# Kernel tuning notes

Hardware: AMD Instinct MI355X
Metric: run time of the kernel (lower is better)

## Reference

```python
import jax, jax.numpy as jnp
import numpy as np

D_MODEL = 1024
N_HEADS = 16
D_FF = 4096
B = 8
S_TGT = 1024
S_SRC = 1024


def layer_norm(x, g, b, eps=1e-5):
    mu = jnp.mean(x, axis=-1, keepdims=True)
    var = jnp.mean(jnp.square(x - mu), axis=-1, keepdims=True)
    return (x - mu) * jax.lax.rsqrt(var + eps) * g + b


def mha(q_in, k_in, v_in, Wq, bq, Wk, bk, Wv, bv, Wo, bo, mask):
    Bq, Sq, D = q_in.shape
    hd = D // N_HEADS

    def split(t):
        return t.reshape(t.shape[0], t.shape[1], N_HEADS, hd).transpose(0, 2, 1, 3)

    Q = split(q_in @ Wq + bq)   # [B,H,Sq,hd]
    K = split(k_in @ Wk + bk)   # [B,H,Sk,hd]
    V = split(v_in @ Wv + bv)
    scores = jnp.einsum('bhqd,bhkd->bhqk', Q, K) / jnp.sqrt(jnp.float32(hd))
    scores = jnp.where(mask, scores, jnp.float32(-1e9))
    attn = jax.nn.softmax(scores, axis=-1)
    out = jnp.einsum('bhqk,bhkd->bhqd', attn, V)
    out = out.transpose(0, 2, 1, 3).reshape(Bq, Sq, D)
    return out @ Wo + bo


def setup_inputs() -> dict:
    key = jax.random.key(0)
    ks = jax.random.split(key, 32)
    s = 0.02
    inp = {
        'x': jax.random.normal(ks[0], (B, S_TGT, D_MODEL), dtype=jnp.float32),
        'encoder_output': jax.random.normal(ks[1], (B, S_SRC, D_MODEL), dtype=jnp.float32),
        'tgt_mask': jnp.tril(jnp.ones((S_TGT, S_TGT), dtype=bool))[None, None],
        'src_mask': jnp.ones((1, 1, S_TGT, S_SRC), dtype=bool),
    }
    i = 2
    for p in ('sa', 'ca'):
        for w in ('Wq', 'Wk', 'Wv', 'Wo'):
            inp[f'{p}_{w}'] = jax.random.normal(ks[i], (D_MODEL, D_MODEL), dtype=jnp.float32) * s
            inp[f'{p}_b{w[1].lower()}'] = jnp.zeros((D_MODEL,), dtype=jnp.float32)
            i += 1
    inp['ff_W1'] = jax.random.normal(ks[i], (D_MODEL, D_FF), dtype=jnp.float32) * s; i += 1
    inp['ff_b1'] = jnp.zeros((D_FF,), dtype=jnp.float32)
    inp['ff_W2'] = jax.random.normal(ks[i], (D_FF, D_MODEL), dtype=jnp.float32) * s; i += 1
    inp['ff_b2'] = jnp.zeros((D_MODEL,), dtype=jnp.float32)
    for n in ('ln1', 'ln2', 'ln3'):
        inp[f'{n}_g'] = jnp.ones((D_MODEL,), dtype=jnp.float32)
        inp[f'{n}_b'] = jnp.zeros((D_MODEL,), dtype=jnp.float32)
    return inp


def reference(x, encoder_output, tgt_mask, src_mask,
              sa_Wq, sa_bq, sa_Wk, sa_bk, sa_Wv, sa_bv, sa_Wo, sa_bo,
              ca_Wq, ca_bq, ca_Wk, ca_bk, ca_Wv, ca_bv, ca_Wo, ca_bo,
              ff_W1, ff_b1, ff_W2, ff_b2,
              ln1_g, ln1_b, ln2_g, ln2_b, ln3_g, ln3_b):
    # masked self-attention + residual + LN (dropout = identity in eval mode)
    attn = mha(x, x, x, sa_Wq, sa_bq, sa_Wk, sa_bk, sa_Wv, sa_bv, sa_Wo, sa_bo, tgt_mask)
    x = layer_norm(x + attn, ln1_g, ln1_b)
    # cross-attention to encoder output
    cross = mha(x, encoder_output, encoder_output,
                ca_Wq, ca_bq, ca_Wk, ca_bk, ca_Wv, ca_bv, ca_Wo, ca_bo, src_mask)
    x = layer_norm(x + cross, ln2_g, ln2_b)
    # position-wise FFN: Linear -> ReLU -> Linear
    ff = jax.nn.relu(x @ ff_W1 + ff_b1) @ ff_W2 + ff_b2
    x = layer_norm(x + ff, ln3_g, ln3_b)
    return x
```

## Files before the change

kernel.cpp:

```cpp
#include <hip/hip_runtime.h>
#include <math.h>

typedef __attribute__((ext_vector_type(8))) short short8;
typedef __attribute__((ext_vector_type(4))) short short4v;
typedef __attribute__((ext_vector_type(4))) float floatx4;
typedef __attribute__((ext_vector_type(16))) float floatx16;

__device__ inline float bf2f(unsigned short h) {
    unsigned int u = ((unsigned int)h) << 16;
    float f;
    __builtin_memcpy(&f, &u, 4);
    return f;
}
__device__ inline unsigned short f2bf(float f) {
    unsigned int u;
    __builtin_memcpy(&u, &f, 4);
    u = (u + 0x7fffu + ((u >> 16) & 1u)) >> 16;
    return (unsigned short)u;
}
__device__ inline unsigned int f2u(float f) {
    return __builtin_bit_cast(unsigned int, f);
}
__device__ inline float exp2_raw(float x) {
    float r;
    asm("v_exp_f32 %0, %1" : "=v"(r) : "v"(x));
    return r;
}

__device__ inline void gld_lds16(const unsigned short* g, unsigned short* l) {
    __builtin_amdgcn_global_load_lds(
        (const __attribute__((address_space(1))) unsigned int*)g,
        (__attribute__((address_space(3))) unsigned int*)l, 16, 0, 0);
}

__global__ __launch_bounds__(256) void detect_dtype(
    const unsigned short* __restrict__ x, int* __restrict__ flag) {
    __shared__ int s[4];
    int bad = 0;
    for (int i = threadIdx.x; i < 8192; i += 256) {
        float v = bf2f(x[i]);
        if (!(fabsf(v) <= 1.0e4f)) bad = 1;
    }
    unsigned long long b = __ballot(bad);
    int wave = threadIdx.x >> 6;
    if ((threadIdx.x & 63) == 0) s[wave] = (b != 0ULL) ? 1 : 0;
    __syncthreads();
    if (threadIdx.x == 0) flag[0] = s[0] | s[1] | s[2] | s[3];
}

__global__ __launch_bounds__(256) void to_bf16_kernel(
    const void* __restrict__ in, unsigned short* __restrict__ out,
    const int* __restrict__ flag, int n8) {
    int fl = flag[0];
    int i = blockIdx.x * 256 + threadIdx.x;
    if (i >= n8) return;
    size_t off = (size_t)i * 8;
    if (fl) {
        floatx4 f0 = *(const floatx4*)((const float*)in + off);
        floatx4 f1 = *(const floatx4*)((const float*)in + off + 4);
        short8 v;
#pragma unroll
        for (int j = 0; j < 4; j++) {
            v[j] = (short)f2bf(f0[j]);
            v[4 + j] = (short)f2bf(f1[j]);
        }
        *(short8*)(out + off) = v;
    } else {
        *(short8*)(out + off) = *(const short8*)((const unsigned short*)in + off);
    }
}

__global__ __launch_bounds__(256) void transpose_any(
    const void* __restrict__ in, unsigned short* __restrict__ out,
    int rows, int cols, const int* __restrict__ flag) {
    int fl = flag ? flag[0] : 0;
    __shared__ unsigned short t[32][33];
    int tx = threadIdx.x & 31, ty = threadIdx.x >> 5;
    int c0 = blockIdx.x * 32, r0 = blockIdx.y * 32;
    size_t base = (size_t)blockIdx.z * rows * cols;
#pragma unroll
    for (int k = 0; k < 4; k++) {
        size_t idx = base + (size_t)(r0 + ty + k * 8) * cols + c0 + tx;
        t[ty + k * 8][tx] = fl ? f2bf(((const float*)in)[idx])
                               : ((const unsigned short*)in)[idx];
    }
    __syncthreads();
#pragma unroll
    for (int k = 0; k < 4; k++)
        out[base + (size_t)(c0 + ty + k * 8) * rows + r0 + tx] = t[tx][ty + k * 8];
}

struct Ptr8 { const void* p[8]; };
__global__ __launch_bounds__(256) void transpose8(
    Ptr8 in, unsigned short* __restrict__ out, const int* __restrict__ flag) {
    int fl = flag[0];
    __shared__ unsigned short t[32][33];
    const void* src = in.p[blockIdx.z];
    unsigned short* dst = out + (size_t)blockIdx.z * 1024 * 1024;
    int tx = threadIdx.x & 31, ty = threadIdx.x >> 5;
    int c0 = blockIdx.x * 32, r0 = blockIdx.y * 32;
#pragma unroll
    for (int k = 0; k < 4; k++) {
        size_t idx = (size_t)(r0 + ty + k * 8) * 1024 + c0 + tx;
        t[ty + k * 8][tx] = fl ? f2bf(((const float*)src)[idx])
                               : ((const unsigned short*)src)[idx];
    }
    __syncthreads();
#pragma unroll
    for (int k = 0; k < 4; k++)
        dst[(size_t)(c0 + ty + k * 8) * 1024 + r0 + tx] = t[tx][ty + k * 8];
}

__device__ inline void stage_half(const unsigned short* __restrict__ G, int ldk,
                                  int grow, int gcol, unsigned short* ldsb,
                                  int tid) {
    int s0 = tid, s1 = tid + 512;
    int r0 = s0 >> 3, c0 = ((s0 & 7) ^ (r0 & 7)) << 3;
    int r1 = s1 >> 3, c1 = ((s1 & 7) ^ (r1 & 7)) << 3;
    gld_lds16(&G[(size_t)(grow + r0) * ldk + gcol + c0], &ldsb[s0 * 8]);
    gld_lds16(&G[(size_t)(grow + r1) * ldk + gcol + c1], &ldsb[s1 * 8]);
}

template <int BN_, int EPI>
__global__ __launch_bounds__(512) void gemm8(
    const unsigned short* __restrict__ A, const unsigned short* __restrict__ Bt,
    const void* __restrict__ b0, const void* __restrict__ b1,
    const void* __restrict__ b2, unsigned short* __restrict__ C0,
    unsigned short* __restrict__ C1, unsigned short* __restrict__ C2,
    int M, int N, int K, const int* __restrict__ flag) {
    constexpr int NR = BN_ / 64;
    constexpr int WNT = BN_ / 4;
    constexpr int ASZ = 16384;
    constexpr int BSZ = BN_ * 64;
    __shared__ alignas(16) unsigned short lds[2 * ASZ + 2 * BSZ];

    const int tid = threadIdx.x;
    const int lane = tid & 63, wave = tid >> 6;
    const int quad = lane >> 4, l16 = lane & 15, x7 = l16 & 7;
    const int wm = wave >> 2, wn = wave & 3;
    const int bm = blockIdx.x * 256, bn = blockIdx.y * BN_;
    const int NT = K >> 6;

    floatx4 acc[8][NR];
#pragma unroll
    for (int i = 0; i < 8; ++i)
#pragma unroll
        for (int j = 0; j < NR; ++j) acc[i][j] = (floatx4){0.f, 0.f, 0.f, 0.f};

    stage_half(A, K, bm, 0, lds, tid);
    stage_half(A, K, bm + 128, 0, lds + 8192, tid);
    stage_half(Bt, K, bn, 0, lds + 2 * ASZ, tid);
    if (BN_ == 256) stage_half(Bt, K, bn + 128, 0, lds + 2 * ASZ + 8192, tid);
    asm volatile("s_waitcnt vmcnt(0)" ::: "memory");
    __builtin_amdgcn_s_barrier();

    short8 bfr[NR][2], afr[2][2][2];

    for (int it = 0; it < NT; ++it) {
        unsigned short* const Ac = lds + (it & 1) * ASZ;
        unsigned short* const Bc = lds + 2 * ASZ + (it & 1) * BSZ;
        unsigned short* const An = lds + ((it + 1) & 1) * ASZ;
        unsigned short* const Bn = lds + 2 * ASZ + ((it + 1) & 1) * BSZ;
        const bool more = (it + 1 < NT);
        if (more) {
            const int kn = (it + 1) << 6;
            stage_half(A, K, bm, kn, An, tid);
            stage_half(A, K, bm + 128, kn, An + 8192, tid);
            stage_half(Bt, K, bn, kn, Bn, tid);
            if (BN_ == 256) stage_half(Bt, K, bn + 128, kn, Bn + 8192, tid);
        }
#pragma unroll
        for (int ni = 0; ni < NR; ++ni)
#pragma unroll
            for (int ks = 0; ks < 2; ++ks)
                bfr[ni][ks] = *(const short8*)&Bc[
                    (wn * WNT + ni * 16 + l16) * 64 +
                    ((((ks << 2) + quad) ^ x7) << 3)];
#pragma unroll
        for (int m2 = 0; m2 < 2; ++m2)
#pragma unroll
            for (int ks = 0; ks < 2; ++ks)
                afr[0][m2][ks] = *(const short8*)&Ac[
                    (wm * 128 + m2 * 16 + l16) * 64 +
                    ((((ks << 2) + quad) ^ x7) << 3)];
#pragma unroll
        for (int q = 0; q < 4; ++q) {
            if (q < 3) {
#pragma unroll
                for (int m2 = 0; m2 < 2; ++m2)
#pragma unroll
                    for (int ks = 0; ks < 2; ++ks)
                        afr[(q + 1) & 1][m2][ks] = *(const short8*)&Ac[
                            (wm * 128 + ((q + 1) * 2 + m2) * 16 + l16) * 64 +
                            ((((ks << 2) + quad) ^ x7) << 3)];
            }
            __builtin_amdgcn_s_setprio(1);
#pragma unroll
            for (int m2 = 0; m2 < 2; ++m2)
#pragma unroll
                for (int ni = 0; ni < NR; ++ni) {
                    acc[q * 2 + m2][ni] = __builtin_amdgcn_mfma_f32_16x16x32_bf16(
                        bfr[ni][0], afr[q & 1][m2][0], acc[q * 2 + m2][ni], 0, 0, 0);
                    acc[q * 2 + m2][ni] = __builtin_amdgcn_mfma_f32_16x16x32_bf16(
                        bfr[ni][1], afr[q & 1][m2][1], acc[q * 2 + m2][ni], 0, 0, 0);
                }
            __builtin_amdgcn_s_setprio(0);
        }
        if (more) {
            asm volatile("s_waitcnt vmcnt(0)" ::: "memory");
            __builtin_amdgcn_s_barrier();
        }
    }

    const int fl = flag[0];
    const void* bp = b0;
    unsigned short* Cp = C0;
    int mode = 0;
    int cb = bn;
    if (EPI == 1) mode = 1;
    if (EPI == 4) mode = 2;
    if (EPI == 2) {
        int ch = bn >> 10;
        cb = bn & 1023;
        bp = (ch == 0) ? b0 : (ch == 1) ? b1 : b2;
        Cp = (ch == 0) ? C0 : (ch == 1) ? C1 : C2;
        mode = (ch == 0) ? 2 : (ch == 1) ? 3 : 4;
    }
    if (EPI == 3) {
        int ch = bn >> 10;
        cb = bn & 1023;
        bp = (ch == 0) ? b0 : b1;
        Cp = (ch == 0) ? C0 : C1;
        mode = (ch == 0) ? 3 : 4;
    }

    if (mode == 4) {
#pragma unroll
        for (int ni = 0; ni < NR; ++ni) {
            const int colb = cb + wn * WNT + ni * 16 + quad * 4;
            float b4[4];
            if (fl) {
                floatx4 t = *(const floatx4*)&((const float*)bp)[colb];
#pragma unroll
                for (int r = 0; r < 4; ++r) b4[r] = t[r];
            } else {
                short4v t = *(const short4v*)&((const unsigned short*)bp)[colb];
#pragma unroll
                for (int r = 0; r < 4; ++r) b4[r] = bf2f((unsigned short)t[r]);
            }
            const int hh = colb >> 6, dd = colb & 63;
#pragma unroll
            for (int mi = 0; mi < 8; ++mi) {
                const int row = bm + wm * 128 + mi * 16 + l16;
                const int b_ = row >> 10, s_ = row & 1023;
#pragma unroll
                for (int r = 0; r < 4; ++r) {
                    float v = acc[mi][ni][r] + b4[r];
                    Cp[(((size_t)b_ * 16 + hh) * 64 + dd + r) * 1024 + s_] = f2bf(v);
                }
            }
        }
    } else {
        constexpr int SLOTS = WNT / 8;
        constexpr int SMASK = SLOTS - 1;
        __syncthreads();
        unsigned short* W2 = lds + wave * (128 * WNT);
#pragma unroll
        for (int ni = 0; ni < NR; ++ni) {
            const int colb = cb + wn * WNT + ni * 16 + quad * 4;
            float b4[4];
            if (fl) {
                floatx4 t = *(const floatx4*)&((const float*)bp)[colb];
#pragma unroll
                for (int r = 0; r < 4; ++r) b4[r] = t[r];
            } else {
                short4v t = *(const short4v*)&((const unsigned short*)bp)[colb];
#pragma unroll
                for (int r = 0; r < 4; ++r) b4[r] = bf2f((unsigned short)t[r]);
            }
            const int cslot = ni * 2 + (quad >> 1);
            const int chalf = quad & 1;
#pragma unroll
            for (int mi = 0; mi < 8; ++mi) {
                const int r = mi * 16 + l16;
                short4v pk;
#pragma unroll
                for (int rr = 0; rr < 4; ++rr) {
                    float v = acc[mi][ni][rr] + b4[rr];
                    if (mode == 1) v = fmaxf(v, 0.f);
                    if (mode == 2) v *= 0.18033688f;
                    pk[rr] = (short)f2bf(v);
                }
                *(short4v*)&W2[r * WNT + ((cslot ^ (r & SMASK)) << 3) +
                               (chalf << 2)] = pk;
            }
        }
        const int lslot = lane & SMASK;
        const int lrow = lane / SLOTS;
        constexpr int RPP = 64 / SLOTS;
#pragma unroll
        for (int p = 0; p < 128 / RPP; ++p) {
            const int r = p * RPP + lrow;
            short8 v = *(const short8*)&W2[r * WNT + ((lslot ^ (r & SMASK)) << 3)];
            const int colg = cb + wn * WNT + (lslot << 3);
            const int rowg = bm + wm * 128 + r;
            if (mode <= 1) {
                *(short8*)&Cp[(size_t)rowg * N + colg] = v;
            } else {
                const int b_ = rowg >> 10, s_ = rowg & 1023;
                const int hh2 = colg >> 6, dd2 = colg & 63;
                *(short8*)&Cp[((((size_t)b_ * 16 + hh2) * 1024) + s_) * 64 + dd2] = v;
            }
        }
    }
}

template <int CAUSAL>
__global__ __launch_bounds__(256) void attn_kernel(
    const unsigned short* __restrict__ Q, const unsigned short* __restrict__ K,
    const unsigned short* __restrict__ Vt, unsigned short* __restrict__ O,
    int Skv) {
    __shared__ alignas(16) unsigned short Ks[2][512 * 8];
    __shared__ alignas(16) unsigned short Vs[2][512 * 8];
    const int S = 1024;
    int tid = threadIdx.x, wave = tid >> 6, lane = tid & 63;
    int h = lane >> 5, l31 = lane & 31;
    int fid = blockIdx.y * 8 + blockIdx.x;
    int bh = fid & 127;
    int qt = fid >> 7;
    if (CAUSAL) qt = 7 - qt;
    const int qb = qt * 128 + wave * 32;
    const unsigned short* Qp = Q + (size_t)bh * S * 64;
    const unsigned short* Kp = K + (size_t)bh * Skv * 64;
    const unsigned short* Vp = Vt + (size_t)bh * 64 * Skv;

    short8 qf[4];
#pragma unroll
    for (int t = 0; t < 4; t++)
        qf[t] = *(const short8*)&Qp[(qb + l31) * 64 + t * 16 + h * 8];

    floatx16 o[2];
#pragma unroll
    for (int dn = 0; dn < 2; dn++)
#pragma unroll
        for (int rr = 0; rr < 16; rr++) o[dn][rr] = 0.f;
    float m = -1e30f, l = 0.f;
    const int kend = CAUSAL ? (qt + 1) * 128 : Skv;
    const int nch = kend >> 6;

    int sr0 = tid >> 3, sc0 = (tid & 7) ^ (sr0 & 7);
    int sr1 = (tid + 256) >> 3, sc1 = ((tid + 256) & 7) ^ (sr1 & 7);

    auto stageKV = [&](int kb, int b) {
        gld_lds16(&Kp[(size_t)(kb + sr0) * 64 + sc0 * 8], &Ks[b][tid * 8]);
        gld_lds16(&Kp[(size_t)(kb + sr1) * 64 + sc1 * 8], &Ks[b][(tid + 256) * 8]);
        gld_lds16(&Vp[(size_t)sr0 * Skv + kb + sc0 * 8], &Vs[b][tid * 8]);
        gld_lds16(&Vp[(size_t)sr1 * Skv + kb + sc1 * 8], &Vs[b][(tid + 256) * 8]);
    };

    stageKV(0, 0);
    asm volatile("s_waitcnt vmcnt(0)" ::: "memory");
    __builtin_amdgcn_s_barrier();

    for (int ic = 0; ic < nch; ++ic) {
        const int kb = ic << 6, cur = ic & 1;
        const unsigned short* Ksc = Ks[cur];
        const unsigned short* Vsc = Vs[cur];
        if (ic + 1 < nch) stageKV(kb + 64, cur ^ 1);

        const bool act = !CAUSAL || (kb <= qb + 31);
        if (act) {
            floatx16 st[2];
            __builtin_amdgcn_s_setprio(1);
#pragma unroll
            for (int kg = 0; kg < 2; kg++) {
                const int row = kg * 32 + l31, r7 = row & 7;
                floatx16 z;
#pragma unroll
                for (int rr = 0; rr < 16; rr++) z[rr] = 0.f;
#pragma unroll
                for (int t = 0; t < 4; t++) {
                    short8 kf = *(const short8*)&Ksc[
                        (row * 8 + ((2 * t + h) ^ r7)) * 8];
                    z = __builtin_amdgcn_mfma_f32_32x32x16_bf16(kf, qf[t], z,
                                                                0, 0, 0);
                }
                st[kg] = z;
            }
            __builtin_amdgcn_s_setprio(0);

            if (CAUSAL && (kb + 63 > qb)) {
#pragma unroll
                for (int kg = 0; kg < 2; kg++)
#pragma unroll
                    for (int rr = 0; rr < 16; rr++) {
                        int key = kb + kg * 32 + (rr & 3) + 8 * (rr >> 2) + 4 * h;
                        if (key > qb + l31) st[kg][rr] = -1e30f;
                    }
            }
            float mx[16];
#pragma unroll
            for (int rr = 0; rr < 16; rr++) mx[rr] = fmaxf(st[0][rr], st[1][rr]);
#pragma unroll
            for (int s2 = 8; s2 > 0; s2 >>= 1)
#pragma unroll
                for (int rr = 0; rr < s2; rr++)
                    mx[rr] = fmaxf(mx[rr], mx[rr + s2]);
            float smax = fmaxf(mx[0], __shfl_xor(mx[0], 32));
            float mi = m;
            if (!__all(smax <= m + 8.f)) {
                mi = fmaxf(m, smax);
                float alpha = exp2_raw(m - mi);
                l *= alpha;
#pragma unroll
                for (int dn = 0; dn < 2; dn++)
#pragma unroll
                    for (int rr = 0; rr < 16; rr++) o[dn][rr] *= alpha;
                m = mi;
            }
#pragma unroll
            for (int kg = 0; kg < 2; kg++)
#pragma unroll
                for (int rr = 0; rr < 16; rr++)
                    st[kg][rr] = exp2_raw(st[kg][rr] - mi);
            float sm[16];
#pragma unroll
            for (int rr = 0; rr < 16; rr++) sm[rr] = st[0][rr] + st[1][rr];
#pragma unroll
            for (int s2 = 8; s2 > 0; s2 >>= 1)
#pragma unroll
                for (int rr = 0; rr < s2; rr++) sm[rr] += sm[rr + s2];
            l += sm[0] + __shfl_xor(sm[0], 32);

            unsigned int pd[2][4][2];
#pragma unroll
            for (int kg = 0; kg < 2; kg++)
#pragma unroll
                for (int g = 0; g < 4; g++)
#pragma unroll
                    for (int i = 0; i < 2; i++)
                        pd[kg][g][i] = __builtin_amdgcn_perm(
                            f2u(st[kg][4 * g + 2 * i + 1]),
                            f2u(st[kg][4 * g + 2 * i]), 0x07060302u);

            __builtin_amdgcn_s_setprio(1);
#pragma unroll
            for (int kg = 0; kg < 2; kg++)
#pragma unroll
                for (int kt = 0; kt < 2; kt++) {
                    unsigned int dw[4];
#pragma unroll
                    for (int i = 0; i < 2; i++) {
                        unsigned int a = pd[kg][2 * kt][i];
                        unsigned int b_ = pd[kg][2 * kt + 1][i];
                        unsigned int ax = (unsigned int)__shfl_xor((int)a, 32);
                        unsigned int bx = (unsigned int)__shfl_xor((int)b_, 32);
                        dw[i] = h ? bx : a;
                        dw[2 + i] = h ? b_ : ax;
                    }
                    short8 pf;
                    __builtin_memcpy(&pf, dw, 16);
#pragma unroll
                    for (int dn = 0; dn < 2; dn++) {
                        const int row = dn * 32 + l31, r7 = row & 7;
                        short8 vf = *(const short8*)&Vsc[
                            (row * 8 + ((kg * 4 + 2 * kt + h) ^ r7)) * 8];
                        o[dn] = __builtin_amdgcn_mfma_f32_32x32x16_bf16(
                            vf, pf, o[dn], 0, 0, 0);
                    }
                }
            __builtin_amdgcn_s_setprio(0);
        }

        if (ic + 1 < nch) {
            asm volatile("s_waitcnt vmcnt(0)" ::: "memory");
            __builtin_amdgcn_s_barrier();
        }
    }

    int b = bh >> 4, hh = bh & 15;
    float inv = 1.0f / l;
    size_t orow = ((size_t)(b * S + qb + l31)) * 1024 + hh * 64;
#pragma unroll
    for (int dn = 0; dn < 2; dn++)
#pragma unroll
        for (int g = 0; g < 4; g++) {
            short4v p4;
#pragma unroll
            for (int r = 0; r < 4; r++)
                p4[r] = (short)f2bf(o[dn][4 * g + r] * inv);
            *(short4v*)&O[orow + dn * 32 + 8 * g + 4 * h] = p4;
        }
}

template <int AEXT, int OEXT>
__global__ __launch_bounds__(256) void add_ln_kernel(
    const void* __restrict__ A, const unsigned short* __restrict__ Bv,
    const void* __restrict__ g, const void* __restrict__ be,
    void* __restrict__ out, const int* __restrict__ flag) {
    int fl = flag[0];
    __shared__ float red[2][4];
    int row = blockIdx.x, tid = threadIdx.x;
    size_t base = (size_t)row * 1024;
    int c = tid * 4;
    float v[4], sum = 0.f, ss = 0.f;
    if (AEXT && fl) {
        floatx4 af = *(const floatx4*)&((const float*)A)[base + c];
#pragma unroll
        for (int k = 0; k < 4; k++) v[k] = af[k];
    } else {
        short4v av = *(const short4v*)&((const unsigned short*)A)[base + c];
#pragma unroll
        for (int k = 0; k < 4; k++) v[k] = bf2f((unsigned short)av[k]);
    }
    short4v bv = *(const short4v*)&Bv[base + c];
#pragma unroll
    for (int k = 0; k < 4; k++) {
        v[k] += bf2f((unsigned short)bv[k]);
        sum += v[k];
        ss += v[k] * v[k];
    }
#pragma unroll
    for (int off = 1; off < 64; off <<= 1) {
        sum += __shfl_xor(sum, off);
        ss += __shfl_xor(ss, off);
    }
    int wave = tid >> 6, lane = tid & 63;
    if (lane == 0) {
        red[0][wave] = sum;
        red[1][wave] = ss;
    }
    __syncthreads();
    sum = red[0][0] + red[0][1] + red[0][2] + red[0][3];
    ss = red[1][0] + red[1][1] + red[1][2] + red[1][3];
    float mu = sum * (1.0f / 1024.0f);
    float var = ss * (1.0f / 1024.0f) - mu * mu;
    float rstd = rsqrtf(var + 1e-5f);
#pragma unroll
    for (int k = 0; k < 4; k++) {
        float gv = fl ? ((const float*)g)[c + k]
                      : bf2f(((const unsigned short*)g)[c + k]);
        float bev = fl ? ((const float*)be)[c + k]
                       : bf2f(((const unsigned short*)be)[c + k]);
        float y = (v[k] - mu) * rstd * gv + bev;
        if (OEXT && fl)
            ((float*)out)[base + c + k] = y;
        else
            ((unsigned short*)out)[base + c + k] = f2bf(y);
    }
}

extern "C" void kernel_launch(void* const* d_in, const int* in_sizes, int n_in,
                              void* d_out, int out_size, void* d_ws, size_t ws_size,
                              hipStream_t stream) {
    const int M = 8192;
    typedef const void* cvp;
    cvp x = d_in[0];
    cvp enc = d_in[1];
    cvp saWq = d_in[4], sabq = d_in[5];
    cvp saWk = d_in[6], sabk = d_in[7];
    cvp saWv = d_in[8], sabv = d_in[9];
    cvp saWo = d_in[10], sabo = d_in[11];
    cvp caWq = d_in[12], cabq = d_in[13];
    cvp caWk = d_in[14], cabk = d_in[15];
    cvp caWv = d_in[16], cabv = d_in[17];
    cvp caWo = d_in[18], cabo = d_in[19];
    cvp ffW1 = d_in[20], ffb1 = d_in[21];
    cvp ffW2 = d_in[22], ffb2 = d_in[23];
    cvp ln1g = d_in[24], ln1b = d_in[25];
    cvp ln2g = d_in[26], ln2b = d_in[27];
    cvp ln3g = d_in[28], ln3b = d_in[29];

    char* ws = (char*)d_ws;
    const size_t MB = 1024 * 1024;
    typedef unsigned short* up;
    up wt_sa_qkv = (up)(ws + 0);
    up wt_sa_o   = (up)(ws + 6 * MB);
    up wt_ca_q   = (up)(ws + 8 * MB);
    up wt_ca_kv  = (up)(ws + 10 * MB);
    up wt_ca_o   = (up)(ws + 14 * MB);
    up wtff1     = (up)(ws + 16 * MB);
    up wtff2     = (up)(ws + 24 * MB);
    up Qb  = (up)(ws + 32 * MB);
    up Kb  = (up)(ws + 48 * MB);
    up Vtb = (up)(ws + 64 * MB);
    up xb  = (up)(ws + 80 * MB);
    up Hb  = (up)(ws + 32 * MB);
    up Ob  = (up)(ws + 96 * MB);
    up Pb  = (up)(ws + 112 * MB);
    up x1  = (up)(ws + 128 * MB);
    up x2  = (up)(ws + 144 * MB);
    up encb = (up)(ws + 144 * MB);
    int* flag = (int*)(ws + 160 * MB);

    dim3 blk(256), blk5(512);
    detect_dtype<<<1, blk, 0, stream>>>((const unsigned short*)x, flag);

    to_bf16_kernel<<<4096, blk, 0, stream>>>(x, xb, flag, M * 1024 / 8);
    to_bf16_kernel<<<4096, blk, 0, stream>>>(enc, encb, flag, M * 1024 / 8);

    Ptr8 w8;
    w8.p[0] = saWq; w8.p[1] = saWk; w8.p[2] = saWv; w8.p[3] = saWo;
    w8.p[4] = caWq; w8.p[5] = caWk; w8.p[6] = caWv; w8.p[7] = caWo;
    transpose8<<<dim3(32, 32, 8), blk, 0, stream>>>(w8, (up)(ws + 0), flag);
    transpose_any<<<dim3(128, 32, 1), blk, 0, stream>>>(ffW1, wtff1, 1024, 4096, flag);
    transpose_any<<<dim3(32, 128, 1), blk, 0, stream>>>(ffW2, wtff2, 4096, 1024, flag);

    gemm8<256, 2><<<dim3(32, 12), blk5, 0, stream>>>(
        xb, wt_sa_qkv, sabq, sabk, sabv, Qb, Kb, Vtb, M, 3072, 1024, flag);
    attn_kernel<1><<<dim3(8, 128), blk, 0, stream>>>(Qb, Kb, Vtb, Ob, 1024);
    gemm8<128, 0><<<dim3(32, 8), blk5, 0, stream>>>(
        Ob, wt_sa_o, sabo, nullptr, nullptr, Pb, nullptr, nullptr, M, 1024, 1024, flag);
    add_ln_kernel<1, 0><<<dim3(8192), blk, 0, stream>>>(x, Pb, ln1g, ln1b, x1, flag);

    gemm8<128, 4><<<dim3(32, 8), blk5, 0, stream>>>(
        x1, wt_ca_q, cabq, nullptr, nullptr, Qb, nullptr, nullptr, M, 1024, 1024, flag);
    gemm8<256, 3><<<dim3(32, 8), blk5, 0, stream>>>(
        encb, wt_ca_kv, cabk, cabv, nullptr, Kb, Vtb, nullptr, M, 2048, 1024, flag);
    attn_kernel<0><<<dim3(8, 128), blk, 0, stream>>>(Qb, Kb, Vtb, Ob, 1024);
    gemm8<128, 0><<<dim3(32, 8), blk5, 0, stream>>>(
        Ob, wt_ca_o, cabo, nullptr, nullptr, Pb, nullptr, nullptr, M, 1024, 1024, flag);
    add_ln_kernel<0, 0><<<dim3(8192), blk, 0, stream>>>(x1, Pb, ln2g, ln2b, x2, flag);

    gemm8<256, 1><<<dim3(32, 16), blk5, 0, stream>>>(
        x2, wtff1, ffb1, nullptr, nullptr, Hb, nullptr, nullptr, M, 4096, 1024, flag);
    gemm8<128, 0><<<dim3(32, 8), blk5, 0, stream>>>(
        Hb, wtff2, ffb2, nullptr, nullptr, Pb, nullptr, nullptr, M, 1024, 4096, flag);
    add_ln_kernel<0, 1><<<dim3(8192), blk, 0, stream>>>(x2, Pb, ln3g, ln3b, d_out, flag);
}
```

Before: 703.4 us.

## Add 128x128 gemm4 for N=1024 GEMMs, MFMA row-sum in attention, merge bf16 casts

Adds a new 256-thread 128x128-tile GEMM with 16x16x32 MFMAs and uses it for the four N=1024 projections. The goal is a larger grid (512 blocks instead of 256) to fill more CUs. The attention kernel computes the softmax row sum with MFMAs against a ones vector instead of a shuffle reduction, and flattens the max reduction tree. The two input bf16 conversions are merged into a single launch. Costs include extra MFMA work for the sum and a smaller per-block tile, which means less data reuse.

```diff
diff --git a/kernel.cpp b/kernel.cpp
--- a/kernel.cpp
+++ b/kernel.cpp
@@ -48,10 +48,13 @@
     if (threadIdx.x == 0) flag[0] = s[0] | s[1] | s[2] | s[3];
 }
 
-__global__ __launch_bounds__(256) void to_bf16_kernel(
-    const void* __restrict__ in, unsigned short* __restrict__ out,
+__global__ __launch_bounds__(256) void to_bf16_2(
+    const void* __restrict__ inA, const void* __restrict__ inB,
+    unsigned short* __restrict__ outA, unsigned short* __restrict__ outB,
     const int* __restrict__ flag, int n8) {
     int fl = flag[0];
+    const void* in = blockIdx.z ? inB : inA;
+    unsigned short* out = blockIdx.z ? outB : outA;
     int i = blockIdx.x * 256 + threadIdx.x;
     if (i >= n8) return;
     size_t off = (size_t)i * 8;
@@ -311,6 +314,134 @@
                 const int hh2 = colg >> 6, dd2 = colg & 63;
                 *(short8*)&Cp[((((size_t)b_ * 16 + hh2) * 1024) + s_) * 64 + dd2] = v;
             }
+        }
+    }
+}
+
+__device__ inline void stage128(const unsigned short* __restrict__ G, int ldk,
+                                int grow, int gcol, unsigned short* ldsb,
+                                int tid) {
+#pragma unroll
+    for (int p = 0; p < 4; ++p) {
+        int s = p * 256 + tid;
+        int r = s >> 3, c = ((s & 7) ^ (r & 7)) << 3;
+        gld_lds16(&G[(size_t)(grow + r) * ldk + gcol + c], &ldsb[s * 8]);
+    }
+}
+
+template <int EPI>
+__global__ __launch_bounds__(256) void gemm4(
+    const unsigned short* __restrict__ A, const unsigned short* __restrict__ Bt,
+    const void* __restrict__ bias, unsigned short* __restrict__ C,
+    int M, int N, int K, const int* __restrict__ flag) {
+    constexpr int TSZ = 8192;
+    __shared__ alignas(16) unsigned short lds[4 * TSZ];
+
+    const int tid = threadIdx.x;
+    const int lane = tid & 63, wave = tid >> 6;
+    const int quad = lane >> 4, l16 = lane & 15, x7 = l16 & 7;
+    const int wm = wave >> 1, wn = wave & 1;
+    const int bm = blockIdx.x * 128, bn = blockIdx.y * 128;
+    const int NT = K >> 6;
+
+    floatx4 acc[4][4];
+#pragma unroll
+    for (int i = 0; i < 4; ++i)
+#pragma unroll
+        for (int j = 0; j < 4; ++j) acc[i][j] = (floatx4){0.f, 0.f, 0.f, 0.f};
+
+    stage128(A, K, bm, 0, lds, tid);
+    stage128(Bt, K, bn, 0, lds + 2 * TSZ, tid);
+    asm volatile("s_waitcnt vmcnt(0)" ::: "memory");
+    __builtin_amdgcn_s_barrier();
+
+    short8 afr[4][2], bfr[4][2];
+    for (int it = 0; it < NT; ++it) {
+        unsigned short* const Ac = lds + (it & 1) * TSZ;
+        unsigned short* const Bc = lds + 2 * TSZ + (it & 1) * TSZ;
+        const bool more = (it + 1 < NT);
+        if (more) {
+            const int kn = (it + 1) << 6;
+            stage128(A, K, bm, kn, lds + ((it + 1) & 1) * TSZ, tid);
+            stage128(Bt, K, bn, kn, lds + 2 * TSZ + ((it + 1) & 1) * TSZ, tid);
+        }
+#pragma unroll
+        for (int ni = 0; ni < 4; ++ni)
+#pragma unroll
+            for (int ks = 0; ks < 2; ++ks)
+                bfr[ni][ks] = *(const short8*)&Bc[
+                    (wn * 64 + ni * 16 + l16) * 64 +
+                    ((((ks << 2) + quad) ^ x7) << 3)];
+#pragma unroll
+        for (int mi = 0; mi < 4; ++mi)
+#pragma unroll
+            for (int ks = 0; ks < 2; ++ks)
+                afr[mi][ks] = *(const short8*)&Ac[
+                    (wm * 64 + mi * 16 + l16) * 64 +
+                    ((((ks << 2) + quad) ^ x7) << 3)];
+        __builtin_amdgcn_s_setprio(1);
+#pragma unroll
+        for (int mi = 0; mi < 4; ++mi)
+#pragma unroll
+            for (int ni = 0; ni < 4; ++ni) {
+                acc[mi][ni] = __builtin_amdgcn_mfma_f32_16x16x32_bf16(
+                    bfr[ni][0], afr[mi][0], acc[mi][ni], 0, 0, 0);
+                acc[mi][ni] = __builtin_amdgcn_mfma_f32_16x16x32_bf16(
+                    bfr[ni][1], afr[mi][1], acc[mi][ni], 0, 0, 0);
+            }
+        __builtin_amdgcn_s_setprio(0);
+        if (more) {
+            asm volatile("s_waitcnt vmcnt(0)" ::: "memory");
+            __builtin_amdgcn_s_barrier();
+        }
+    }
+
+    const int fl = flag[0];
+    constexpr int mode = (EPI == 1) ? 1 : (EPI == 4) ? 2 : 0;
+    __syncthreads();
+    unsigned short* W2 = lds + wave * 4096;
+#pragma unroll
+    for (int ni = 0; ni < 4; ++ni) {
+        const int colb = bn + wn * 64 + ni * 16 + quad * 4;
+        float b4[4];
+        if (fl) {
+            floatx4 t = *(const floatx4*)&((const float*)bias)[colb];
+#pragma unroll
+            for (int r = 0; r < 4; ++r) b4[r] = t[r];
+        } else {
+            short4v t = *(const short4v*)&((const unsigned short*)bias)[colb];
+#pragma unroll
+            for (int r = 0; r < 4; ++r) b4[r] = bf2f((unsigned short)t[r]);
+        }
+        const int cslot = ni * 2 + (quad >> 1);
+        const int chalf = quad & 1;
+#pragma unroll
+        for (int mi = 0; mi < 4; ++mi) {
+            const int r = mi * 16 + l16;
+            short4v pk;
+#pragma unroll
+            for (int rr = 0; rr < 4; ++rr) {
+                float v = acc[mi][ni][rr] + b4[rr];
+                if (mode == 1) v = fmaxf(v, 0.f);
+                if (mode == 2) v *= 0.18033688f;
+                pk[rr] = (short)f2bf(v);
+            }
+            *(short4v*)&W2[r * 64 + ((cslot ^ (r & 7)) << 3) + (chalf << 2)] = pk;
+        }
+    }
+    const int lslot = lane & 7, lrow = lane >> 3;
+#pragma unroll
+    for (int p = 0; p < 8; ++p) {
+        const int r = p * 8 + lrow;
+        short8 v = *(const short8*)&W2[r * 64 + ((lslot ^ (r & 7)) << 3)];
+        const int colg = bn + wn * 64 + (lslot << 3);
+        const int rowg = bm + wm * 64 + r;
+        if (mode <= 1) {
+            *(short8*)&C[(size_t)rowg * N + colg] = v;
+        } else {
+            const int b_ = rowg >> 10, s_ = rowg & 1023;
+            const int hh = colg >> 6, dd = colg & 63;
+            *(short8*)&C[((((size_t)b_ * 16 + hh) * 1024) + s_) * 64 + dd] = v;
         }
     }
 }
@@ -340,16 +471,25 @@
         qf[t] = *(const short8*)&Qp[(qb + l31) * 64 + t * 16 + h * 8];
 
     floatx16 o[2];
-#pragma unroll
-    for (int dn = 0; dn < 2; dn++)
-#pragma unroll
-        for (int rr = 0; rr < 16; rr++) o[dn][rr] = 0.f;
+    floatx16 fz;
+#pragma unroll
+    for (int rr = 0; rr < 16; rr++) {
+        o[0][rr] = 0.f;
+        o[1][rr] = 0.f;
+        fz[rr] = 0.f;
+    }
     float m = -1e30f, l = 0.f;
     const int kend = CAUSAL ? (qt + 1) * 128 : Skv;
     const int nch = kend >> 6;
 
     int sr0 = tid >> 3, sc0 = (tid & 7) ^ (sr0 & 7);
     int sr1 = (tid + 256) >> 3, sc1 = ((tid + 256) & 7) ^ (sr1 & 7);
+
+    short8 vone;
+    {
+        unsigned int dw[4] = {0x3F803F80u, 0x3F803F80u, 0x3F803F80u, 0x3F803F80u};
+        __builtin_memcpy(&vone, dw, 16);
+    }
 
     auto stageKV = [&](int kb, int b) {
         gld_lds16(&Kp[(size_t)(kb + sr0) * 64 + sc0 * 8], &Ks[b][tid * 8]);
@@ -375,9 +515,7 @@
 #pragma unroll
             for (int kg = 0; kg < 2; kg++) {
                 const int row = kg * 32 + l31, r7 = row & 7;
-                floatx16 z;
-#pragma unroll
-                for (int rr = 0; rr < 16; rr++) z[rr] = 0.f;
+                floatx16 z = fz;
 #pragma unroll
                 for (int t = 0; t < 4; t++) {
                     short8 kf = *(const short8*)&Ksc[
@@ -398,15 +536,22 @@
                         if (key > qb + l31) st[kg][rr] = -1e30f;
                     }
             }
-            float mx[16];
-#pragma unroll
-            for (int rr = 0; rr < 16; rr++) mx[rr] = fmaxf(st[0][rr], st[1][rr]);
-#pragma unroll
-            for (int s2 = 8; s2 > 0; s2 >>= 1)
-#pragma unroll
-                for (int rr = 0; rr < s2; rr++)
-                    mx[rr] = fmaxf(mx[rr], mx[rr + s2]);
-            float smax = fmaxf(mx[0], __shfl_xor(mx[0], 32));
+            float a0 = fmaxf(st[0][0], st[1][0]), a1 = fmaxf(st[0][1], st[1][1]);
+            float a2 = fmaxf(st[0][2], st[1][2]), a3 = fmaxf(st[0][3], st[1][3]);
+            float a4 = fmaxf(st[0][4], st[1][4]), a5 = fmaxf(st[0][5], st[1][5]);
+            float a6 = fmaxf(st[0][6], st[1][6]), a7 = fmaxf(st[0][7], st[1][7]);
+            float a8 = fmaxf(st[0][8], st[1][8]), a9 = fmaxf(st[0][9], st[1][9]);
+            float aa = fmaxf(st[0][10], st[1][10]), ab = fmaxf(st[0][11], st[1][11]);
+            float ac = fmaxf(st[0][12], st[1][12]), ad = fmaxf(st[0][13], st[1][13]);
+            float ae = fmaxf(st[0][14], st[1][14]), af = fmaxf(st[0][15], st[1][15]);
+            float t0 = fmaxf(fmaxf(a0, a1), a2);
+            float t1 = fmaxf(fmaxf(a3, a4), a5);
+            float t2 = fmaxf(fmaxf(a6, a7), a8);
+            float t3 = fmaxf(fmaxf(a9, aa), ab);
+            float t4 = fmaxf(fmaxf(ac, ad), ae);
+            float smax = fmaxf(fmaxf(fmaxf(t0, t1), fmaxf(t2, t3)),
+                               fmaxf(t4, af));
+            smax = fmaxf(smax, __shfl_xor(smax, 32));
             float mi = m;
             if (!__all(smax <= m + 8.f)) {
                 mi = fmaxf(m, smax);
@@ -423,14 +568,6 @@
 #pragma unroll
                 for (int rr = 0; rr < 16; rr++)
                     st[kg][rr] = exp2_raw(st[kg][rr] - mi);
-            float sm[16];
-#pragma unroll
-            for (int rr = 0; rr < 16; rr++) sm[rr] = st[0][rr] + st[1][rr];
-#pragma unroll
-            for (int s2 = 8; s2 > 0; s2 >>= 1)
-#pragma unroll
-                for (int rr = 0; rr < s2; rr++) sm[rr] += sm[rr + s2];
-            l += sm[0] + __shfl_xor(sm[0], 32);
 
             unsigned int pd[2][4][2];
 #pragma unroll
@@ -443,7 +580,7 @@
                             f2u(st[kg][4 * g + 2 * i + 1]),
                             f2u(st[kg][4 * g + 2 * i]), 0x07060302u);
 
-            __builtin_amdgcn_s_setprio(1);
+            short8 pf[2][2];
 #pragma unroll
             for (int kg = 0; kg < 2; kg++)
 #pragma unroll
@@ -458,17 +595,30 @@
                         dw[i] = h ? bx : a;
                         dw[2 + i] = h ? b_ : ax;
                     }
-                    short8 pf;
-                    __builtin_memcpy(&pf, dw, 16);
+                    __builtin_memcpy(&pf[kg][kt], dw, 16);
+                }
+
+            __builtin_amdgcn_s_setprio(1);
+            {
+                floatx16 zs = __builtin_amdgcn_mfma_f32_32x32x16_bf16(
+                    vone, pf[0][0], fz, 0, 0, 0);
+                zs = __builtin_amdgcn_mfma_f32_32x32x16_bf16(vone, pf[0][1], zs, 0, 0, 0);
+                zs = __builtin_amdgcn_mfma_f32_32x32x16_bf16(vone, pf[1][0], zs, 0, 0, 0);
+                zs = __builtin_amdgcn_mfma_f32_32x32x16_bf16(vone, pf[1][1], zs, 0, 0, 0);
+                l += zs[0];
+            }
+#pragma unroll
+            for (int kg = 0; kg < 2; kg++)
+#pragma unroll
+                for (int kt = 0; kt < 2; kt++)
 #pragma unroll
                     for (int dn = 0; dn < 2; dn++) {
                         const int row = dn * 32 + l31, r7 = row & 7;
                         short8 vf = *(const short8*)&Vsc[
                             (row * 8 + ((kg * 4 + 2 * kt + h) ^ r7)) * 8];
                         o[dn] = __builtin_amdgcn_mfma_f32_32x32x16_bf16(
-                            vf, pf, o[dn], 0, 0, 0);
+                            vf, pf[kg][kt], o[dn], 0, 0, 0);
                     }
-                }
             __builtin_amdgcn_s_setprio(0);
         }
 
@@ -596,8 +746,8 @@
     dim3 blk(256), blk5(512);
     detect_dtype<<<1, blk, 0, stream>>>((const unsigned short*)x, flag);
 
-    to_bf16_kernel<<<4096, blk, 0, stream>>>(x, xb, flag, M * 1024 / 8);
-    to_bf16_kernel<<<4096, blk, 0, stream>>>(enc, encb, flag, M * 1024 / 8);
+    to_bf16_2<<<dim3(4096, 1, 2), blk, 0, stream>>>(x, enc, xb, encb, flag,
+                                                    M * 1024 / 8);
 
     Ptr8 w8;
     w8.p[0] = saWq; w8.p[1] = saWk; w8.p[2] = saWv; w8.p[3] = saWo;
@@ -609,22 +759,22 @@
     gemm8<256, 2><<<dim3(32, 12), blk5, 0, stream>>>(
         xb, wt_sa_qkv, sabq, sabk, sabv, Qb, Kb, Vtb, M, 3072, 1024, flag);
     attn_kernel<1><<<dim3(8, 128), blk, 0, stream>>>(Qb, Kb, Vtb, Ob, 1024);
-    gemm8<128, 0><<<dim3(32, 8), blk5, 0, stream>>>(
-        Ob, wt_sa_o, sabo, nullptr, nullptr, Pb, nullptr, nullptr, M, 1024, 1024, flag);
+    gemm4<0><<<dim3(64, 8), blk, 0, stream>>>(
+        Ob, wt_sa_o, sabo, Pb, M, 1024, 1024, flag);
     add_ln_kernel<1, 0><<<dim3(8192), blk, 0, stream>>>(x, Pb, ln1g, ln1b, x1, flag);
 
-    gemm8<128, 4><<<dim3(32, 8), blk5, 0, stream>>>(
-        x1, wt_ca_q, cabq, nullptr, nullptr, Qb, nullptr, nullptr, M, 1024, 1024, flag);
+    gemm4<4><<<dim3(64, 8), blk, 0, stream>>>(
+        x1, wt_ca_q, cabq, Qb, M, 1024, 1024, flag);
     gemm8<256, 3><<<dim3(32, 8), blk5, 0, stream>>>(
         encb, wt_ca_kv, cabk, cabv, nullptr, Kb, Vtb, nullptr, M, 2048, 1024, flag);
     attn_kernel<0><<<dim3(8, 128), blk, 0, stream>>>(Qb, Kb, Vtb, Ob, 1024);
-    gemm8<128, 0><<<dim3(32, 8), blk5, 0, stream>>>(
-        Ob, wt_ca_o, cabo, nullptr, nullptr, Pb, nullptr, nullptr, M, 1024, 1024, flag);
+    gemm4<0><<<dim3(64, 8), blk, 0, stream>>>(
+        Ob, wt_ca_o, cabo, Pb, M, 1024, 1024, flag);
     add_ln_kernel<0, 0><<<dim3(8192), blk, 0, stream>>>(x1, Pb, ln2g, ln2b, x2, flag);
 
     gemm8<256, 1><<<dim3(32, 16), blk5, 0, stream>>>(
         x2, wtff1, ffb1, nullptr, nullptr, Hb, nullptr, nullptr, M, 4096, 1024, flag);
-    gemm8<128, 0><<<dim3(32, 8), blk5, 0, stream>>>(
-        Hb, wtff2, ffb2, nullptr, nullptr, Pb, nullptr, nullptr, M, 1024, 4096, flag);
+    gemm4<0><<<dim3(64, 8), blk, 0, stream>>>(
+        Hb, wtff2, ffb2, Pb, M, 1024, 4096, flag);
     add_ln_kernel<0, 1><<<dim3(8192), blk, 0, stream>>>(x2, Pb, ln3g, ln3b, d_out, flag);
 }
```

After: 716.4 us. Within noise of the previous version (+1.8%).
